# Performance work log

Measured on AMD Instinct MI355X. Metric: run time of the kernel, lower is better.

Reference implementation:

```python
import jax, jax.numpy as jnp
import numpy as np

N, E = 50000, 800000
IN_C, HID_C, OUT_C, HEADS = 128, 32, 16, 4
NEG_SLOPE = 0.2


def gat_conv(x, src, dst, W, att_src, att_dst, bias, heads, out_ch, concat, n_nodes):
    # linear transform: [N, heads, out_ch]
    h = (x @ W).reshape(n_nodes, heads, out_ch)
    # per-node attention logits [N, heads]
    a_s = (h * att_src).sum(-1)
    a_d = (h * att_dst).sum(-1)
    # per-edge raw attention (edge j->i uses src logit of j, dst logit of i)
    alpha = jax.nn.leaky_relu(a_s[src] + a_d[dst], negative_slope=NEG_SLOPE)  # [E, heads]
    # segment softmax over destination neighborhoods
    amax = jax.ops.segment_max(alpha, dst, num_segments=n_nodes)
    ex = jnp.exp(alpha - amax[dst])
    den = jax.ops.segment_sum(ex, dst, num_segments=n_nodes)
    coef = ex / den[dst]  # [E, heads]
    # weighted scatter-add aggregation
    msg = h[src] * coef[:, :, None]  # [E, heads, out_ch]
    out = jax.ops.segment_sum(msg, dst, num_segments=n_nodes)  # [N, heads, out_ch]
    out = out.reshape(n_nodes, heads * out_ch) if concat else out.mean(axis=1)
    return out + bias


def setup_inputs() -> dict:
    key = jax.random.key(0)
    ks = jax.random.split(key, 10)
    x = jax.random.normal(ks[0], (N, IN_C), dtype=jnp.float32)
    edge_index = jax.random.randint(ks[1], (2, E), 0, N, dtype=jnp.int64)
    s1 = 1.0 / np.sqrt(IN_C)
    s2 = 1.0 / np.sqrt(HID_C * HEADS)
    W1 = jax.random.normal(ks[2], (IN_C, HEADS * HID_C), dtype=jnp.float32) * s1
    att_src1 = jax.random.normal(ks[3], (HEADS, HID_C), dtype=jnp.float32) * s1
    att_dst1 = jax.random.normal(ks[4], (HEADS, HID_C), dtype=jnp.float32) * s1
    b1 = jnp.zeros((HEADS * HID_C,), dtype=jnp.float32)
    W2 = jax.random.normal(ks[5], (HEADS * HID_C, OUT_C), dtype=jnp.float32) * s2
    att_src2 = jax.random.normal(ks[6], (1, OUT_C), dtype=jnp.float32) * s2
    att_dst2 = jax.random.normal(ks[7], (1, OUT_C), dtype=jnp.float32) * s2
    b2 = jnp.zeros((OUT_C,), dtype=jnp.float32)
    return {"x": x, "edge_index": edge_index, "W1": W1, "att_src1": att_src1,
            "att_dst1": att_dst1, "b1": b1, "W2": W2, "att_src2": att_src2,
            "att_dst2": att_dst2, "b2": b2}


def reference(x, edge_index, W1, att_src1, att_dst1, b1, W2, att_src2, att_dst2, b2):
    n = x.shape[0]
    # PyG GATConv default: add self loops
    ar = jnp.arange(n, dtype=edge_index.dtype)
    src = jnp.concatenate([edge_index[0], ar])
    dst = jnp.concatenate([edge_index[1], ar])
    h = gat_conv(x, src, dst, W1, att_src1, att_dst1, b1, HEADS, HID_C, True, n)
    h = jax.nn.elu(h)
    out = gat_conv(h, src, dst, W2, att_src2, att_dst2, b2, 1, OUT_C, False, n)
    return out
```

## Files before the change

### kernel.cpp

```cpp
#include <hip/hip_runtime.h>

typedef __attribute__((ext_vector_type(8))) short short8;
typedef __attribute__((ext_vector_type(4))) float f32x4;

__device__ __forceinline__ float lrelu02(float a) { return a > 0.0f ? a : 0.2f * a; }

__device__ __forceinline__ unsigned bf16rne(float f) {
    unsigned u = __float_as_uint(f);
    return (u + 0x7fffu + ((u >> 16) & 1u)) >> 16;
}

__global__ __launch_bounds__(256) void k_zero(int4* __restrict__ p, int n4) {
    int i = blockIdx.x * blockDim.x + threadIdx.x;
    if (i < n4) p[i] = make_int4(0, 0, 0, 0);
}

__global__ __launch_bounds__(256) void k_rank(
    const int* __restrict__ ei, int* __restrict__ deg, int* __restrict__ rank,
    int E, int N)
{
    int tid = blockIdx.x * blockDim.x + threadIdx.x;
    int nthr = gridDim.x * blockDim.x;
    int E4 = E & ~3;
    for (int b = tid * 4; b < E4; b += nthr * 4) {
        int4 d = *(const int4*)(ei + E + b);
        int4 r;
        r.x = atomicAdd(&deg[d.x], 1);
        r.y = atomicAdd(&deg[d.y], 1);
        r.z = atomicAdd(&deg[d.z], 1);
        r.w = atomicAdd(&deg[d.w], 1);
        *(int4*)(rank + b) = r;
    }
    for (int e = E4 + tid; e < E; e += nthr)
        rank[e] = atomicAdd(&deg[ei[E + e]], 1);
    for (int i = tid; i < N; i += nthr)
        rank[E + i] = atomicAdd(&deg[i], 1);
}

__global__ __launch_bounds__(256) void k_gemm1(
    const float* __restrict__ x, const float* __restrict__ W,
    const float* __restrict__ attS, const float* __restrict__ attD,
    unsigned short* __restrict__ h1, float* __restrict__ as1, float* __restrict__ ad1, int N)
{
    __shared__ unsigned short Wt[128 * 128];
    __shared__ unsigned short xs[64 * 128];

    const int t = threadIdx.x;
    const int lane = t & 63;
    const int wv = t >> 6;
    const int ln = lane & 15;
    const int lg = lane >> 4;
    const int r0 = blockIdx.x * 64;

    #pragma unroll
    for (int i = 0; i < 16; ++i) {
        int flat = i * 256 + t;
        int n = flat & 127;
        int k0 = (flat >> 7) * 4;
        float v0 = W[(size_t)(k0 + 0) * 128 + n];
        float v1 = W[(size_t)(k0 + 1) * 128 + n];
        float v2 = W[(size_t)(k0 + 2) * 128 + n];
        float v3 = W[(size_t)(k0 + 3) * 128 + n];
        uint2 pk;
        pk.x = bf16rne(v0) | (bf16rne(v1) << 16);
        pk.y = bf16rne(v2) | (bf16rne(v3) << 16);
        int byteo = n * 256 + ((k0 * 2) ^ ((n & 7) << 4));
        *(uint2*)((char*)Wt + byteo) = pk;
    }
    {
        int mbase = t >> 5, k0 = (t & 31) * 4;
        #pragma unroll
        for (int it = 0; it < 8; ++it) {
            int m = mbase + it * 8;
            int rr = r0 + m;
            float4 v = make_float4(0.f, 0.f, 0.f, 0.f);
            if (rr < N) v = *(const float4*)&x[(size_t)rr * 128 + k0];
            unsigned lo = bf16rne(v.x) | (bf16rne(v.y) << 16);
            unsigned hi = bf16rne(v.z) | (bf16rne(v.w) << 16);
            int byteo = m * 256 + ((k0 * 2) ^ ((m & 7) << 4));
            *(uint2*)((char*)xs + byteo) = make_uint2(lo, hi);
        }
    }
    __syncthreads();

    f32x4 acc[8];
    #pragma unroll
    for (int i = 0; i < 8; ++i) acc[i] = (f32x4)(0.f);

    #pragma unroll
    for (int kk = 0; kk < 4; ++kk) {
        int kb = (kk * 32 + lg * 8) * 2;
        int am = wv * 16 + ln;
        short8 a = *(const short8*)((char*)xs + am * 256 + (kb ^ ((am & 7) << 4)));
        #pragma unroll
        for (int tile = 0; tile < 8; ++tile) {
            int n = tile * 16 + ln;
            short8 b = *(const short8*)((char*)Wt + n * 256 + (kb ^ ((n & 7) << 4)));
            acc[tile] = __builtin_amdgcn_mfma_f32_16x16x32_bf16(a, b, acc[tile], 0, 0, 0);
        }
    }

    float aSt[8], aDt[8];
    #pragma unroll
    for (int tile = 0; tile < 8; ++tile) {
        aSt[tile] = attS[tile * 16 + ln];
        aDt[tile] = attD[tile * 16 + ln];
    }
    #pragma unroll
    for (int r = 0; r < 4; ++r) {
        int row = r0 + wv * 16 + lg * 4 + r;
        #pragma unroll
        for (int h = 0; h < 4; ++h) {
            float s = acc[2*h][r] * aSt[2*h] + acc[2*h+1][r] * aSt[2*h+1];
            float d = acc[2*h][r] * aDt[2*h] + acc[2*h+1][r] * aDt[2*h+1];
            s += __shfl_xor(s, 1); s += __shfl_xor(s, 2); s += __shfl_xor(s, 4); s += __shfl_xor(s, 8);
            d += __shfl_xor(d, 1); d += __shfl_xor(d, 2); d += __shfl_xor(d, 4); d += __shfl_xor(d, 8);
            if (ln == h * 4 + r && row < N) {
                as1[row * 4 + h] = s;
                ad1[row * 4 + h] = d;
            }
        }
    }

    __syncthreads();
    #pragma unroll
    for (int tile = 0; tile < 8; ++tile) {
        #pragma unroll
        for (int r = 0; r < 4; ++r) {
            int m = wv * 16 + lg * 4 + r;
            int byteo = m * 256 + (((tile * 16 + ln) * 2) ^ ((m & 7) << 4));
            *(unsigned short*)((char*)xs + byteo) = (unsigned short)bf16rne(acc[tile][r]);
        }
    }
    __syncthreads();
    #pragma unroll
    for (int it = 0; it < 4; ++it) {
        int idx = t + it * 256;
        int m = idx >> 4, o = idx & 15;
        int byteo = m * 256 + ((o * 16) ^ ((m & 7) << 4));
        if (r0 + m < N)
            *(uint4*)((char*)(h1 + (size_t)(r0 + m) * 128) + o * 16) =
                *(const uint4*)((const char*)xs + byteo);
    }
}

__global__ __launch_bounds__(256) void k_scan_local(
    const int* __restrict__ deg, int* __restrict__ rowptr, int* __restrict__ bsum, int N)
{
    const int t = threadIdx.x;
    const int base = blockIdx.x * 2048 + t * 8;
    int v[8];
    int s = 0;
    #pragma unroll
    for (int j = 0; j < 8; ++j) {
        int idx = base + j;
        v[j] = (idx < N) ? deg[idx] : 0;
        s += v[j];
    }
    __shared__ int ts[256];
    ts[t] = s;
    __syncthreads();
    #pragma unroll
    for (int off = 1; off < 256; off <<= 1) {
        int u = (t >= off) ? ts[t - off] : 0;
        __syncthreads();
        ts[t] += u;
        __syncthreads();
    }
    int ex = (t == 0) ? 0 : ts[t - 1];
    #pragma unroll
    for (int j = 0; j < 8; ++j) {
        int idx = base + j;
        if (idx < N) rowptr[idx] = ex;
        ex += v[j];
    }
    if (t == 255) bsum[blockIdx.x] = ts[255];
}

__global__ __launch_bounds__(256) void k_scan_add(
    int* __restrict__ rowptr, const int* __restrict__ bsum, int N, int ET)
{
    const int t = threadIdx.x;
    __shared__ int soff;
    if (t < 64) {
        int v = (t < (int)blockIdx.x) ? bsum[t] : 0;
        #pragma unroll
        for (int m = 32; m >= 1; m >>= 1) v += __shfl_xor(v, m);
        if (t == 0) soff = v;
    }
    __syncthreads();
    int off = soff;
    const int base = blockIdx.x * 2048 + t * 8;
    #pragma unroll
    for (int j = 0; j < 8; ++j) {
        int idx = base + j;
        if (idx < N) rowptr[idx] += off;
    }
    if (blockIdx.x == 0 && t == 0) rowptr[N] = ET;
}

__global__ __launch_bounds__(256) void k_fill2(const int* __restrict__ ei,
                                               const int* __restrict__ rank,
                                               const int* __restrict__ rowptr,
                                               int* __restrict__ col, int E, int N) {
    int tid = blockIdx.x * blockDim.x + threadIdx.x;
    int nthr = gridDim.x * blockDim.x;
    int E4 = E & ~3;
    for (int b = tid * 4; b < E4; b += nthr * 4) {
        int4 d = *(const int4*)(ei + E + b);
        int4 s = *(const int4*)(ei + b);
        int4 r = *(const int4*)(rank + b);
        col[rowptr[d.x] + r.x] = s.x;
        col[rowptr[d.y] + r.y] = s.y;
        col[rowptr[d.z] + r.z] = s.z;
        col[rowptr[d.w] + r.w] = s.w;
    }
    for (int e = E4 + tid; e < E; e += nthr)
        col[rowptr[ei[E + e]] + rank[e]] = ei[e];
    for (int i = tid; i < N; i += nthr)
        col[rowptr[i] + rank[E + i]] = i;
}

__global__ __launch_bounds__(256) void k_agg1(
    const unsigned short* __restrict__ h1, const float* __restrict__ as1,
    const float* __restrict__ ad1, const int* __restrict__ rowptr,
    const int* __restrict__ col, const float* __restrict__ b1,
    unsigned short* __restrict__ out1, int N)
{
    int wid = (int)(((unsigned)blockIdx.x * blockDim.x + threadIdx.x) >> 6);
    if (wid >= N) return;
    int lane = threadIdx.x & 63;
    int start = rowptr[wid], end = rowptr[wid + 1];
    int deg = end - start;
    const float4 ad = *(const float4*)(ad1 + (size_t)wid * 4);
    int head = lane >> 4;
    float adh = head == 0 ? ad.x : head == 1 ? ad.y : head == 2 ? ad.z : ad.w;

    float acc0 = 0.f, acc1 = 0.f;

    if (deg <= 64) {
        int idx = lane & 15;
        float ex[4];
        float den = 0.f;
        #pragma unroll
        for (int b = 0; b < 4; ++b) {
            int j = b * 16 + idx;
            float v = 0.f;
            if (j < deg) {
                int src = col[start + j];
                v = __expf(lrelu02(as1[(size_t)src * 4 + head] + adh));
            }
            ex[b] = v;
            den += v;
        }
        den += __shfl_xor(den, 1); den += __shfl_xor(den, 2);
        den += __shfl_xor(den, 4); den += __shfl_xor(den, 8);
        float rden = 1.f / den;
        #pragma unroll
        for (int b = 0; b < 4; ++b) ex[b] *= rden;
        int srcbase = lane & 48;
        #pragma unroll
        for (int b = 0; b < 4; ++b) {
            if (b * 16 >= deg) break;
            int sq[16]; float cf[16]; unsigned hv[16];
            #pragma unroll
            for (int q = 0; q < 16; ++q) {
                int j = b * 16 + q;
                sq[q] = __builtin_amdgcn_readfirstlane(col[start + (j < deg ? j : 0)]);
                cf[q] = __shfl(ex[b], srcbase | q);
            }
            #pragma unroll
            for (int q = 0; q < 16; ++q)
                hv[q] = *(const unsigned*)(h1 + (size_t)sq[q] * 128 + lane * 2);
            #pragma unroll
            for (int q = 0; q < 16; ++q) {
                acc0 = fmaf(cf[q], __uint_as_float(hv[q] << 16), acc0);
                acc1 = fmaf(cf[q], __uint_as_float(hv[q] & 0xffff0000u), acc1);
            }
        }
    } else {
        float den0 = 0.f, den1 = 0.f, den2 = 0.f, den3 = 0.f;
        for (int e = start + lane; e < end; e += 64) {
            int src = col[e];
            const float4 a = *(const float4*)(as1 + (size_t)src * 4);
            den0 += __expf(lrelu02(a.x + ad.x));
            den1 += __expf(lrelu02(a.y + ad.y));
            den2 += __expf(lrelu02(a.z + ad.z));
            den3 += __expf(lrelu02(a.w + ad.w));
        }
        #pragma unroll
        for (int m = 32; m >= 1; m >>= 1) {
            den0 += __shfl_xor(den0, m); den1 += __shfl_xor(den1, m);
            den2 += __shfl_xor(den2, m); den3 += __shfl_xor(den3, m);
        }
        float rden = head == 0 ? 1.f/den0 : head == 1 ? 1.f/den1 : head == 2 ? 1.f/den2 : 1.f/den3;
        for (int e = start; e < end; e += 8) {
            int sq[8]; float av[8], km[8]; unsigned hv[8];
            #pragma unroll
            for (int j = 0; j < 8; ++j) {
                int ee = e + j;
                bool ok = ee < end;
                int es = ok ? ee : e;
                sq[j] = __builtin_amdgcn_readfirstlane(col[es]);
                km[j] = ok ? 1.f : 0.f;
            }
            #pragma unroll
            for (int j = 0; j < 8; ++j)
                av[j] = as1[(size_t)sq[j] * 4 + head];
            #pragma unroll
            for (int j = 0; j < 8; ++j)
                hv[j] = *(const unsigned*)(h1 + (size_t)sq[j] * 128 + lane * 2);
            #pragma unroll
            for (int j = 0; j < 8; ++j) {
                float coef = km[j] * __expf(lrelu02(av[j] + adh)) * rden;
                acc0 = fmaf(coef, __uint_as_float(hv[j] << 16), acc0);
                acc1 = fmaf(coef, __uint_as_float(hv[j] & 0xffff0000u), acc1);
            }
        }
    }

    int c0 = lane * 2;
    float o0 = acc0 + b1[c0];
    float o1 = acc1 + b1[c0 + 1];
    o0 = o0 > 0.f ? o0 : expm1f(o0);
    o1 = o1 > 0.f ? o1 : expm1f(o1);
    unsigned ov = bf16rne(o0) | (bf16rne(o1) << 16);
    *(unsigned*)((char*)out1 + (size_t)wid * 256 + lane * 4) = ov;
}

__global__ __launch_bounds__(256) void k_gemm2(
    const unsigned short* __restrict__ in, const float* __restrict__ W,
    const float* __restrict__ attS, const float* __restrict__ attD,
    float* __restrict__ h2, float* __restrict__ as2, float* __restrict__ ad2, int N)
{
    __shared__ unsigned short Wt[16 * 128];
    __shared__ unsigned short xs[64 * 128];
    const int t = threadIdx.x;
    const int lane = t & 63;
    const int wv = t >> 6;
    const int ln = lane & 15;
    const int lg = lane >> 4;
    const int r0 = blockIdx.x * 64;

    #pragma unroll
    for (int i = 0; i < 2; ++i) {
        int flat = i * 256 + t;
        int n = flat & 15;
        int k0 = (flat >> 4) * 4;
        float v0 = W[(size_t)(k0 + 0) * 16 + n];
        float v1 = W[(size_t)(k0 + 1) * 16 + n];
        float v2 = W[(size_t)(k0 + 2) * 16 + n];
        float v3 = W[(size_t)(k0 + 3) * 16 + n];
        uint2 pk;
        pk.x = bf16rne(v0) | (bf16rne(v1) << 16);
        pk.y = bf16rne(v2) | (bf16rne(v3) << 16);
        int byteo = n * 256 + ((k0 * 2) ^ ((n & 7) << 4));
        *(uint2*)((char*)Wt + byteo) = pk;
    }
    #pragma unroll
    for (int it = 0; it < 4; ++it) {
        int idx = t + it * 256;
        int m = idx >> 4, o = idx & 15;
        int rr = r0 + m;
        uint4 v = make_uint4(0, 0, 0, 0);
        if (rr < N) v = *(const uint4*)((const char*)(in + (size_t)rr * 128) + o * 16);
        int byteo = m * 256 + ((o * 16) ^ ((m & 7) << 4));
        *(uint4*)((char*)xs + byteo) = v;
    }
    __syncthreads();

    f32x4 acc = (f32x4)(0.f);
    #pragma unroll
    for (int kk = 0; kk < 4; ++kk) {
        int kb = (kk * 32 + lg * 8) * 2;
        int am = wv * 16 + ln;
        short8 a = *(const short8*)((char*)xs + am * 256 + (kb ^ ((am & 7) << 4)));
        short8 b = *(const short8*)((char*)Wt + ln * 256 + (kb ^ ((ln & 7) << 4)));
        acc = __builtin_amdgcn_mfma_f32_16x16x32_bf16(a, b, acc, 0, 0, 0);
    }

    float aSv = attS[ln], aDv = attD[ln];
    #pragma unroll
    for (int r = 0; r < 4; ++r) {
        int row = r0 + wv * 16 + lg * 4 + r;
        float s = acc[r] * aSv;
        float d = acc[r] * aDv;
        s += __shfl_xor(s, 1); s += __shfl_xor(s, 2); s += __shfl_xor(s, 4); s += __shfl_xor(s, 8);
        d += __shfl_xor(d, 1); d += __shfl_xor(d, 2); d += __shfl_xor(d, 4); d += __shfl_xor(d, 8);
        if (row < N) {
            h2[(size_t)row * 16 + ln] = acc[r];
            if (ln == 0) { as2[row] = s; ad2[row] = d; }
        }
    }
}

__global__ __launch_bounds__(256) void k_agg2(
    const float* __restrict__ h2, const float* __restrict__ as2,
    const float* __restrict__ ad2, const int* __restrict__ rowptr,
    const int* __restrict__ col, const float* __restrict__ b2,
    float* __restrict__ out, int N)
{
    int wid = (int)(((unsigned)blockIdx.x * blockDim.x + threadIdx.x) >> 6);
    if (wid >= N) return;
    int lane = threadIdx.x & 63;
    int start = rowptr[wid], end = rowptr[wid + 1];
    int deg = end - start;
    float adv = ad2[wid];
    int sub = lane >> 4, c = lane & 15;
    float acc = 0.f;

    if (deg <= 64) {
        float ex0 = 0.f;
        if (lane < deg) ex0 = __expf(lrelu02(as2[col[start + lane]] + adv));
        float den = ex0;
        #pragma unroll
        for (int m = 32; m >= 1; m >>= 1) den += __shfl_xor(den, m);
        ex0 *= 1.f / den;
        #pragma unroll
        for (int g = 0; g < 4; ++g) {
            if (g * 16 >= deg) break;
            int s[4]; float cf[4], hv[4];
            #pragma unroll
            for (int jj = 0; jj < 4; ++jj) {
                int j = g * 16 + jj * 4 + sub;
                s[jj]  = col[start + (j < deg ? j : 0)];
                cf[jj] = __shfl(ex0, j);
            }
            #pragma unroll
            for (int jj = 0; jj < 4; ++jj)
                hv[jj] = h2[(size_t)s[jj] * 16 + c];
            #pragma unroll
            for (int jj = 0; jj < 4; ++jj)
                acc = fmaf(cf[jj], hv[jj], acc);
        }
    } else {
        float den = 0.f;
        for (int e = start + lane; e < end; e += 64)
            den += __expf(lrelu02(as2[col[e]] + adv));
        #pragma unroll
        for (int m = 32; m >= 1; m >>= 1) den += __shfl_xor(den, m);
        float rden = 1.f / den;
        for (int e0 = start + sub; e0 < end; e0 += 16) {
            int s[4]; float av[4], km[4], hv[4];
            #pragma unroll
            for (int jj = 0; jj < 4; ++jj) {
                int ee = e0 + jj * 4;
                bool ok = ee < end;
                int es = ok ? ee : e0;
                s[jj]  = col[es];
                km[jj] = ok ? 1.f : 0.f;
            }
            #pragma unroll
            for (int jj = 0; jj < 4; ++jj)
                av[jj] = as2[s[jj]];
            #pragma unroll
            for (int jj = 0; jj < 4; ++jj)
                hv[jj] = h2[(size_t)s[jj] * 16 + c];
            #pragma unroll
            for (int jj = 0; jj < 4; ++jj) {
                float coef = km[jj] * __expf(lrelu02(av[jj] + adv)) * rden;
                acc = fmaf(coef, hv[jj], acc);
            }
        }
    }

    acc += __shfl_xor(acc, 16);
    acc += __shfl_xor(acc, 32);
    if (lane < 16) out[(size_t)wid * 16 + lane] = acc + b2[lane];
}

extern "C" void kernel_launch(void* const* d_in, const int* in_sizes, int n_in,
                              void* d_out, int out_size, void* d_ws, size_t ws_size,
                              hipStream_t stream)
{
    const float* x   = (const float*)d_in[0];
    const int*   ei  = (const int*)d_in[1];
    const float* W1  = (const float*)d_in[2];
    const float* aS1 = (const float*)d_in[3];
    const float* aD1 = (const float*)d_in[4];
    const float* b1  = (const float*)d_in[5];
    const float* W2  = (const float*)d_in[6];
    const float* aS2 = (const float*)d_in[7];
    const float* aD2 = (const float*)d_in[8];
    const float* b2  = (const float*)d_in[9];
    float* out = (float*)d_out;

    int N = in_sizes[0] / 128;
    int E = in_sizes[1] / 2;
    int ET = E + N;
    int nblk = (N + 2047) / 2048;
    int G1 = (N + 63) / 64;

    char* w = (char*)d_ws;
    auto alloc = [&](size_t bytes) -> void* {
        void* p = (void*)w;
        w += (bytes + 255) & ~(size_t)255;
        return p;
    };
    unsigned short* h1   = (unsigned short*)alloc((size_t)N * 128 * 2);
    unsigned short* out1 = (unsigned short*)alloc((size_t)N * 128 * 2);
    float* as1   = (float*)alloc((size_t)N * 4 * 4);
    float* ad1   = (float*)alloc((size_t)N * 4 * 4);
    float* h2    = (float*)alloc((size_t)N * 16 * 4);
    float* as2v  = (float*)alloc((size_t)N * 4);
    float* ad2v  = (float*)alloc((size_t)N * 4);
    int* deg     = (int*)alloc((size_t)N * 4);
    int* rowptr  = (int*)alloc((size_t)(N + 1) * 4);
    int* rank    = (int*)alloc((size_t)ET * 4);
    int* col     = (int*)alloc((size_t)ET * 4);
    int* bsum    = (int*)alloc(64 * 4);

    const int tb = 256;
    int n4 = (N + 3) / 4;
    k_zero  <<<(n4 + tb - 1) / tb, tb, 0, stream>>>((int4*)deg, n4);
    k_rank  <<<2048, tb, 0, stream>>>(ei, deg, rank, E, N);
    k_gemm1 <<<G1, tb, 0, stream>>>(x, W1, aS1, aD1, h1, as1, ad1, N);
    k_scan_local<<<nblk, tb, 0, stream>>>(deg, rowptr, bsum, N);
    k_scan_add  <<<nblk, tb, 0, stream>>>(rowptr, bsum, N, ET);
    k_fill2     <<<1024, tb, 0, stream>>>(ei, rank, rowptr, col, E, N);

    k_agg1 <<<(N + 3) / 4, tb, 0, stream>>>(h1, as1, ad1, rowptr, col, b1, out1, N);
    k_gemm2<<<G1, tb, 0, stream>>>(out1, W2, aS2, aD2, h2, as2v, ad2v, N);
    k_agg2 <<<(N + 3) / 4, tb, 0, stream>>>(h2, as2v, ad2v, rowptr, col, b2, out, N);
}
```

Before: 162.5 us.

## Fold degree zeroing into gemm1 and streamline small-degree aggregation gather

Removes the separate zeroing kernel by having k_gemm1 zero the degree array and launching it before k_rank, which saves one launch. In k_agg1's small-degree path, source indices already loaded per lane are broadcast with readlane instead of being reloaded from col with readfirstlane. Partial 16-edge chunks are processed in groups of four so padding edges are no longer gathered. Accumulation uses two-wide float vectors, which may map to packed FMA; the cost is more code and branches.

```diff
diff --git a/kernel.cpp b/kernel.cpp
--- a/kernel.cpp
+++ b/kernel.cpp
@@ -2,17 +2,13 @@
 
 typedef __attribute__((ext_vector_type(8))) short short8;
 typedef __attribute__((ext_vector_type(4))) float f32x4;
+typedef __attribute__((ext_vector_type(2))) float f32x2;
 
 __device__ __forceinline__ float lrelu02(float a) { return a > 0.0f ? a : 0.2f * a; }
 
 __device__ __forceinline__ unsigned bf16rne(float f) {
     unsigned u = __float_as_uint(f);
     return (u + 0x7fffu + ((u >> 16) & 1u)) >> 16;
-}
-
-__global__ __launch_bounds__(256) void k_zero(int4* __restrict__ p, int n4) {
-    int i = blockIdx.x * blockDim.x + threadIdx.x;
-    if (i < n4) p[i] = make_int4(0, 0, 0, 0);
 }
 
 __global__ __launch_bounds__(256) void k_rank(
@@ -40,7 +36,8 @@
 __global__ __launch_bounds__(256) void k_gemm1(
     const float* __restrict__ x, const float* __restrict__ W,
     const float* __restrict__ attS, const float* __restrict__ attD,
-    unsigned short* __restrict__ h1, float* __restrict__ as1, float* __restrict__ ad1, int N)
+    unsigned short* __restrict__ h1, float* __restrict__ as1, float* __restrict__ ad1,
+    int4* __restrict__ degz, int n4, int N)
 {
     __shared__ unsigned short Wt[128 * 128];
     __shared__ unsigned short xs[64 * 128];
@@ -51,6 +48,9 @@
     const int ln = lane & 15;
     const int lg = lane >> 4;
     const int r0 = blockIdx.x * 64;
+
+    for (int i = blockIdx.x * 256 + t; i < n4; i += gridDim.x * 256)
+        degz[i] = make_int4(0, 0, 0, 0);
 
     #pragma unroll
     for (int i = 0; i < 16; ++i) {
@@ -236,20 +236,23 @@
     int head = lane >> 4;
     float adh = head == 0 ? ad.x : head == 1 ? ad.y : head == 2 ? ad.z : ad.w;
 
-    float acc0 = 0.f, acc1 = 0.f;
+    f32x2 acc2 = (f32x2)(0.f);
 
     if (deg <= 64) {
         int idx = lane & 15;
         float ex[4];
+        int sv[4];
         float den = 0.f;
         #pragma unroll
         for (int b = 0; b < 4; ++b) {
             int j = b * 16 + idx;
             float v = 0.f;
+            int sc = 0;
             if (j < deg) {
-                int src = col[start + j];
-                v = __expf(lrelu02(as1[(size_t)src * 4 + head] + adh));
-            }
+                sc = col[start + j];
+                v = __expf(lrelu02(as1[(size_t)sc * 4 + head] + adh));
+            }
+            sv[b] = sc;
             ex[b] = v;
             den += v;
         }
@@ -259,23 +262,50 @@
         #pragma unroll
         for (int b = 0; b < 4; ++b) ex[b] *= rden;
         int srcbase = lane & 48;
+
         #pragma unroll
         for (int b = 0; b < 4; ++b) {
-            if (b * 16 >= deg) break;
-            int sq[16]; float cf[16]; unsigned hv[16];
-            #pragma unroll
-            for (int q = 0; q < 16; ++q) {
-                int j = b * 16 + q;
-                sq[q] = __builtin_amdgcn_readfirstlane(col[start + (j < deg ? j : 0)]);
-                cf[q] = __shfl(ex[b], srcbase | q);
-            }
-            #pragma unroll
-            for (int q = 0; q < 16; ++q)
-                hv[q] = *(const unsigned*)(h1 + (size_t)sq[q] * 128 + lane * 2);
-            #pragma unroll
-            for (int q = 0; q < 16; ++q) {
-                acc0 = fmaf(cf[q], __uint_as_float(hv[q] << 16), acc0);
-                acc1 = fmaf(cf[q], __uint_as_float(hv[q] & 0xffff0000u), acc1);
+            int rem = deg - b * 16;
+            if (rem <= 0) break;
+            if (rem >= 16) {
+                int sq[16]; float cf[16]; unsigned hv[16];
+                #pragma unroll
+                for (int q = 0; q < 16; ++q) {
+                    sq[q] = __builtin_amdgcn_readlane(sv[b], q);
+                    cf[q] = __shfl(ex[b], srcbase | q);
+                }
+                #pragma unroll
+                for (int q = 0; q < 16; ++q)
+                    hv[q] = *(const unsigned*)(h1 + (size_t)sq[q] * 128 + lane * 2);
+                #pragma unroll
+                for (int q = 0; q < 16; ++q) {
+                    f32x2 h2v;
+                    h2v.x = __uint_as_float(hv[q] << 16);
+                    h2v.y = __uint_as_float(hv[q] & 0xffff0000u);
+                    acc2 += (f32x2)(cf[q]) * h2v;
+                }
+            } else {
+                #pragma unroll
+                for (int c4 = 0; c4 < 4; ++c4) {
+                    if (c4 * 4 >= rem) break;
+                    int sq[4]; float cf[4]; unsigned hv[4];
+                    #pragma unroll
+                    for (int jj = 0; jj < 4; ++jj) {
+                        int q = c4 * 4 + jj;
+                        sq[jj] = __builtin_amdgcn_readlane(sv[b], q);
+                        cf[jj] = __shfl(ex[b], srcbase | q);
+                    }
+                    #pragma unroll
+                    for (int jj = 0; jj < 4; ++jj)
+                        hv[jj] = *(const unsigned*)(h1 + (size_t)sq[jj] * 128 + lane * 2);
+                    #pragma unroll
+                    for (int jj = 0; jj < 4; ++jj) {
+                        f32x2 h2v;
+                        h2v.x = __uint_as_float(hv[jj] << 16);
+                        h2v.y = __uint_as_float(hv[jj] & 0xffff0000u);
+                        acc2 += (f32x2)(cf[jj]) * h2v;
+                    }
+                }
             }
         }
     } else {
@@ -313,15 +343,17 @@
             #pragma unroll
             for (int j = 0; j < 8; ++j) {
                 float coef = km[j] * __expf(lrelu02(av[j] + adh)) * rden;
-                acc0 = fmaf(coef, __uint_as_float(hv[j] << 16), acc0);
-                acc1 = fmaf(coef, __uint_as_float(hv[j] & 0xffff0000u), acc1);
+                f32x2 h2v;
+                h2v.x = __uint_as_float(hv[j] << 16);
+                h2v.y = __uint_as_float(hv[j] & 0xffff0000u);
+                acc2 += (f32x2)(coef) * h2v;
             }
         }
     }
 
     int c0 = lane * 2;
-    float o0 = acc0 + b1[c0];
-    float o1 = acc1 + b1[c0 + 1];
+    float o0 = acc2.x + b1[c0];
+    float o1 = acc2.y + b1[c0 + 1];
     o0 = o0 > 0.f ? o0 : expm1f(o0);
     o1 = o1 > 0.f ? o1 : expm1f(o1);
     unsigned ov = bf16rne(o0) | (bf16rne(o1) << 16);
@@ -504,7 +536,7 @@
     float* h2    = (float*)alloc((size_t)N * 16 * 4);
     float* as2v  = (float*)alloc((size_t)N * 4);
     float* ad2v  = (float*)alloc((size_t)N * 4);
-    int* deg     = (int*)alloc((size_t)N * 4);
+    int* deg     = (int*)alloc((size_t)(N + 4) * 4);
     int* rowptr  = (int*)alloc((size_t)(N + 1) * 4);
     int* rank    = (int*)alloc((size_t)ET * 4);
     int* col     = (int*)alloc((size_t)ET * 4);
@@ -512,9 +544,9 @@
 
     const int tb = 256;
     int n4 = (N + 3) / 4;
-    k_zero  <<<(n4 + tb - 1) / tb, tb, 0, stream>>>((int4*)deg, n4);
+
+    k_gemm1 <<<G1, tb, 0, stream>>>(x, W1, aS1, aD1, h1, as1, ad1, (int4*)deg, n4, N);
     k_rank  <<<2048, tb, 0, stream>>>(ei, deg, rank, E, N);
-    k_gemm1 <<<G1, tb, 0, stream>>>(x, W1, aS1, aD1, h1, as1, ad1, N);
     k_scan_local<<<nblk, tb, 0, stream>>>(deg, rowptr, bsum, N);
     k_scan_add  <<<nblk, tb, 0, stream>>>(rowptr, bsum, N, ET);
     k_fill2     <<<1024, tb, 0, stream>>>(ei, rank, rowptr, col, E, N);
```

After: 149.4 us. 8.0% less time.
